# Performance work log

Hardware: AMD Instinct MI355X
Metric: run time of the kernel (lower is better)

Reference implementation:

```python
import jax, jax.numpy as jnp
import numpy as np

D = 768      # embed_dim
L = 8        # depth
NH = 4       # num_heads
HD = D // NH # head_dim = 192
GS = 16      # grid size (max_grid_size)
S = GS * GS  # 256 tokens
B = 64
EPS = 1.1920929e-07  # torch.finfo(float32).eps (RMSNorm eps=None)


def rmsnorm(x):
    return x * jax.lax.rsqrt(jnp.mean(x * x, axis=-1, keepdims=True) + EPS)


def householder_Q(vs):
    # sequential chain of Householder reflections: Q <- Q - (2/||v||^2) v (v^T Q)
    def step(Q, v):
        v = v[:, None]
        Q = Q - (2.0 / (jnp.sum(v * v) + 1e-08)) * (v @ (v.T @ Q))
        return Q, None
    Q, _ = jax.lax.scan(step, jnp.eye(vs.shape[1], dtype=vs.dtype), vs)
    return Q


def setup_inputs() -> dict:
    key = jax.random.key(0)
    ks = jax.random.split(key, 16)
    r = lambda k, shape, s=0.02: jax.random.normal(k, shape, jnp.float32) * s
    return dict(
        z_t=jax.random.normal(ks[0], (B, 3, 32, 32), jnp.float32),
        logsnr=jax.random.normal(ks[1], (B,), jnp.float32),
        qkv_w=r(ks[2], (L, D, 3 * D)),
        out_w=r(ks[3], (L, D, D)),
        gate_w=r(ks[4], (L, D, D)), gate_b=jnp.zeros((L, D), jnp.float32),
        mlpg_w=r(ks[5], (L, D, 8 * D)), mlpg_b=jnp.zeros((L, 8 * D), jnp.float32),
        mlpo_w=r(ks[6], (L, 4 * D, D)), mlpo_b=jnp.zeros((L, D), jnp.float32),
        hh_vs=r(ks[7], (L, HD // 2, HD)),
        patch_w=r(ks[8], (20, D)), patch_b=jnp.zeros((D,), jnp.float32),
        head_w=r(ks[9], (D, 12)), head_b=jnp.zeros((12,), jnp.float32),
        sd1_w=r(ks[10], (8, D)), sd1_b=jnp.zeros((D,), jnp.float32),
        sd2_w=r(ks[11], (D, 12)), sd2_b=jnp.zeros((12,), jnp.float32),
        lam_w=r(ks[12], (D, 1)), lam_b=jnp.zeros((1,), jnp.float32),
    )


def reference(z_t, logsnr, qkv_w, out_w, gate_w, gate_b, mlpg_w, mlpg_b,
              mlpo_w, mlpo_b, hh_vs, patch_w, patch_b, head_w, head_b,
              sd1_w, sd1_b, sd2_w, sd2_b, lam_w, lam_b):
    Bn, C, Him, Wim = z_t.shape
    gh = Him // 2
    # patchify 2x2 -> [B, S, 12]
    patches = z_t.reshape(Bn, C, gh, 2, gh, 2).transpose(0, 2, 4, 1, 3, 5).reshape(Bn, S, 12)
    # FourierFeatures(num_bands=4) -> 8-dim sin/cos embedding of logsnr
    bands = 2.0 ** jnp.arange(4, dtype=jnp.float32)
    ang = logsnr[:, None] * bands
    spins = jnp.concatenate([jnp.sin(ang), jnp.cos(ang)], axis=-1)  # [B, 8]
    x = jnp.concatenate([patches, jnp.broadcast_to(spins[:, None, :], (Bn, S, 8))], axis=-1) @ patch_w + patch_b

    # 2D RoPE tables on the 16x16 grid
    yy, xx = jnp.meshgrid(jnp.arange(GS), jnp.arange(GS), indexing='ij')
    coords = jnp.stack([yy.ravel(), xx.ravel()], axis=1).astype(jnp.float32)  # [S, 2]
    dim_half = HD // 2
    inv_freq = 1.0 / 10000.0 ** (jnp.arange(0, dim_half, 2, dtype=jnp.float32) / dim_half)
    fy = coords[:, 0:1] * inv_freq
    fx = coords[:, 1:2] * inv_freq
    emb = jnp.concatenate([fy, fx, fy, fx], axis=-1)  # [S, HD]
    cos, sin = jnp.cos(emb), jnp.sin(emb)

    # local sliding-window mask: euclidean distance on grid < 2.5
    d2 = jnp.sum((coords[:, None, :] - coords[None, :, :]) ** 2, axis=-1)
    local_mask = d2 < 2.5 ** 2  # [S, S]
    is_glob = jnp.array([(i + 1) % 4 == 0 for i in range(L)])
    scale = 1.0 / jnp.sqrt(jnp.float32(HD))

    def layer(x, p):
        qw, ow, gw, gb, mgw, mgb, mow, mob, vs, glob = p
        h = rmsnorm(x)
        q, k, v = jnp.split(h @ qw, 3, axis=-1)
        heads = lambda t: t.reshape(Bn, S, NH, HD).transpose(0, 2, 1, 3)  # [B,H,S,hd]
        q, k, v = heads(q), heads(k), heads(v)
        # RnRoPE: inverse Householder -> rotate -> forward Householder
        Q = householder_Q(vs)
        q, k = q @ Q.T, k @ Q.T
        def rot(t):
            t1, t2 = jnp.split(t, 2, axis=-1)
            return t * cos + jnp.concatenate([-t2, t1], axis=-1) * sin
        q, k = rot(q) @ Q, rot(k) @ Q
        scores = jnp.einsum('bhqd,bhkd->bhqk', q, k) * scale
        keep = local_mask | glob  # global layers attend everywhere
        scores = jnp.where(keep, scores, -1e30)
        attn = jax.nn.softmax(scores, axis=-1) @ v  # [B,H,S,hd]
        attn = attn.transpose(0, 2, 1, 3).reshape(Bn, S, D) @ ow
        gate = jax.nn.sigmoid(attn @ gw + gb)
        x = x + attn * gate
        g, val = jnp.split(rmsnorm(x) @ mgw + mgb, 2, axis=-1)
        x = x + (val * jax.nn.gelu(g, approximate=False)) @ mow + mob
        return x, None

    x, _ = jax.lax.scan(layer, x, (qkv_w, out_w, gate_w, gate_b, mlpg_w, mlpg_b,
                                   mlpo_w, mlpo_b, hh_vs, is_glob))
    x = rmsnorm(x)
    z_pred = x @ head_w + head_b  # [B, S, 12]
    # factorized mode: FourierScaleDecoder scale and lambda head
    scale_f = jnp.exp(jax.nn.silu(spins @ sd1_w + sd1_b) @ sd2_w + sd2_b)  # [B, 12]
    z_pred = z_pred * scale_f[:, None, :]
    l_pred = (jnp.mean(x, axis=1) @ lam_w + lam_b)[:, 0]
    z_img = z_pred.reshape(Bn, gh, gh, 3, 2, 2).transpose(0, 3, 1, 4, 2, 5).reshape(Bn, C, Him, Wim)
    return z_img, l_pred
```

## Files before the change

kernel.cpp:

```cpp
#include <hip/hip_runtime.h>
#include <hip/hip_bf16.h>
#include <math.h>


#define DEV static __device__ __forceinline__

typedef float    f32x4 __attribute__((ext_vector_type(4)));
typedef short    s16x8 __attribute__((ext_vector_type(8)));
typedef unsigned short u16x8 __attribute__((ext_vector_type(8)));
typedef unsigned short u16x4 __attribute__((ext_vector_type(4)));

constexpr int Bb = 64, Ss = 256, Dd = 768, Ll = 8, NHh = 4, HDd = 192;
constexpr int M_TOK = Bb * Ss;
constexpr float EPS_RMS = 1.1920929e-07f;
constexpr float ATT_SCALE = 0.07216878364870322f;
constexpr size_t ARENA_K = (size_t)Bb * NHh * Ss * HDd;

constexpr size_t B_SPINS  = 0;
constexpr size_t B_SCALEF = 2048;
constexpr size_t B_QT     = 5120;
constexpr size_t B_COS    = B_QT + 1179648;
constexpr size_t B_SIN    = B_COS + 196608;
constexpr size_t B_G      = B_SIN + 196608;
constexpr size_t B_T      = B_G + 294912;
constexpr size_t B_AWY    = B_T + 294912;
constexpr size_t B_ROWLAM = B_AWY + 589824;
constexpr size_t B_X      = B_ROWLAM + 65536;
constexpr size_t B_H      = B_X + 50331648;
constexpr size_t B_PROJ   = B_H + 25165824;
constexpr size_t B_WEFFT  = B_PROJ + 25165824;
constexpr size_t B_OUTWT  = B_WEFFT + 28311552;
constexpr size_t B_GATEWT = B_OUTWT + 9437184;
constexpr size_t B_MLPGT  = B_GATEWT + 9437184;
constexpr size_t B_MLPOT  = B_MLPGT + 75497472;
constexpr size_t B_ARENA  = B_MLPOT + 37748736;

DEV float sigmoidf_(float x) { return 1.0f / (1.0f + expf(-x)); }
DEV float geluf_(float g)    { return 0.5f * g * (1.0f + erff(g * 0.7071067811865476f)); }
DEV unsigned short f2bf(float f) {
    union { float f; unsigned u; } a; a.f = f;
    unsigned u = a.u + 0x7fffu + ((a.u >> 16) & 1u);
    return (unsigned short)(u >> 16);
}
DEV float b2f(unsigned short u) {
    union { unsigned u; float f; } a; a.u = ((unsigned)u) << 16; return a.f;
}
DEV void gload16(const void* g, void* l) {
    __builtin_amdgcn_global_load_lds((const __attribute__((address_space(1))) void*)g,
                                     (__attribute__((address_space(3))) void*)l, 16, 0, 0);
}

DEV void xcd_chunk(int gx, int gy, int CX, int& bx, int& by) {
    int id = by * gx + bx;
    int c = id & 7;
    int s = id >> 3;
    int CY = gy >> 3;
    int subsz = CY * CX;
    int bxc = s / subsz;
    int r = s - bxc * subsz;
    int byl = r / CX;
    by = c * CY + byl;
    bx = bxc * CX + (r - byl * CX);
}

__global__ void spins_kernel(const float* __restrict__ logsnr, float* __restrict__ spins) {
    int b = threadIdx.x;
    if (b < 64) {
        float v = logsnr[b];
#pragma unroll
        for (int j = 0; j < 4; ++j) {
            float ang = v * (float)(1 << j);
            spins[b * 8 + j]     = sinf(ang);
            spins[b * 8 + 4 + j] = cosf(ang);
        }
    }
}

__global__ void rope_table_kernel(float* __restrict__ cosb, float* __restrict__ sinb) {
    int s = blockIdx.x, j = threadIdx.x;
    int y = s >> 4, x = s & 15;
    int base = j % 96;
    float coord, invf;
    if (base < 48) { invf = expf(-(float)base * (2.0f / 96.0f) * 9.210340371976184f); coord = (float)y; }
    else { int i = base - 48; invf = expf(-(float)i * (2.0f / 96.0f) * 9.210340371976184f); coord = (float)x; }
    float f = coord * invf, sv, cv;
    sincosf(f, &sv, &cv);
    cosb[s * 192 + j] = cv;
    sinb[s * 192 + j] = sv;
}

__global__ __launch_bounds__(256) void hh_gram_kernel(const float* __restrict__ hh_vs,
                                                      float* __restrict__ Gm) {
    __shared__ float Y[96][192];
    int l = blockIdx.x, t = threadIdx.x;
    const float4* src = (const float4*)(hh_vs + (size_t)l * 96 * 192);
    for (int i = t; i < 4608; i += 256) ((float4*)&Y[0][0])[i] = src[i];
    __syncthreads();
    for (int e = t; e < 9216; e += 256) {
        int i = e / 96, j = e - (e / 96) * 96;
        float acc = 0.f;
        for (int d = 0; d < 48; ++d) {
            float4 a = *(const float4*)&Y[i][d * 4];
            float4 b = *(const float4*)&Y[j][d * 4];
            acc += a.x * b.x + a.y * b.y + a.z * b.z + a.w * b.w;
        }
        Gm[(size_t)l * 9216 + e] = acc;
    }
}

__global__ __launch_bounds__(128) void hh_t_kernel(const float* __restrict__ Gm,
                                                   float* __restrict__ Tm) {
    __shared__ float G[96][96];
    __shared__ float Tt[96][96];
    int l = blockIdx.x, t = threadIdx.x;
    const float* Gl = Gm + (size_t)l * 9216;
    for (int i = t; i < 9216; i += 128) { ((float*)G)[i] = Gl[i]; ((float*)Tt)[i] = 0.f; }
    __syncthreads();
    if (t < 96) Tt[t][t] = 2.0f / (G[t][t] + 1e-8f);
    __syncthreads();
    for (int j = 1; j < 96; ++j) {
        if (t < 96) {
            float cj = 2.0f / (G[j][j] + 1e-8f);
            float dot = 0.f;
            for (int p = 0; p < j; ++p) dot += Tt[p][t] * G[p][j];
            if (t < j) Tt[j][t] = -cj * dot;
        }
        __syncthreads();
    }
    for (int i = t; i < 9216; i += 128) Tm[(size_t)l * 9216 + i] = ((float*)Tt)[i];
}

__global__ __launch_bounds__(256) void hh_a_kernel(const float* __restrict__ Tm,
                                                   const float* __restrict__ hh_vs,
                                                   float* __restrict__ Am) {
    __shared__ float T[96][96];
    __shared__ float Y[96][192];
    int l = blockIdx.x, t = threadIdx.x;
    const float* Tl = Tm + (size_t)l * 9216;
    const float4* src = (const float4*)(hh_vs + (size_t)l * 96 * 192);
    for (int i = t; i < 9216; i += 256) ((float*)T)[i] = Tl[i];
    for (int i = t; i < 4608; i += 256) ((float4*)&Y[0][0])[i] = src[i];
    __syncthreads();
    for (int idx = t; idx < 4608; idx += 256) {
        int i = idx / 48, e0 = (idx % 48) * 4;
        float4 acc = {0.f, 0.f, 0.f, 0.f};
        for (int j = i; j < 96; ++j) {
            float tv = T[j][i];
            float4 y = *(const float4*)&Y[j][e0];
            acc.x += tv * y.x; acc.y += tv * y.y; acc.z += tv * y.z; acc.w += tv * y.w;
        }
        *(float4*)(Am + (size_t)l * 96 * 192 + (size_t)i * 192 + e0) = acc;
    }
}

__global__ __launch_bounds__(256) void hh_p_kernel(const float* __restrict__ hh_vs,
                                                   const float* __restrict__ Am,
                                                   float* __restrict__ qt) {
    __shared__ float Y[96][192];
    __shared__ float A[96][192];
    int l = blockIdx.x, t = threadIdx.x;
    const float4* ys = (const float4*)(hh_vs + (size_t)l * 96 * 192);
    const float4* as = (const float4*)(Am + (size_t)l * 96 * 192);
    for (int i = t; i < 4608; i += 256) { ((float4*)&Y[0][0])[i] = ys[i]; ((float4*)&A[0][0])[i] = as[i]; }
    __syncthreads();
    for (int idx = t; idx < 9216; idx += 256) {
        int d = idx / 48, e0 = (idx % 48) * 4;
        float4 acc = {0.f, 0.f, 0.f, 0.f};
        for (int i = 0; i < 96; ++i) {
            float yv = Y[i][d];
            float4 a = *(const float4*)&A[i][e0];
            acc.x += yv * a.x; acc.y += yv * a.y; acc.z += yv * a.z; acc.w += yv * a.w;
        }
        acc.x = (d == e0 + 0 ? 1.f : 0.f) - acc.x;
        acc.y = (d == e0 + 1 ? 1.f : 0.f) - acc.y;
        acc.z = (d == e0 + 2 ? 1.f : 0.f) - acc.z;
        acc.w = (d == e0 + 3 ? 1.f : 0.f) - acc.w;
        *(float4*)(qt + (size_t)l * 192 * 192 + (size_t)d * 192 + e0) = acc;
    }
}

__global__ __launch_bounds__(256) void fold_bf16t(const float* __restrict__ qkv_w,
                                                  const float* __restrict__ qt,
                                                  unsigned short* __restrict__ weff_t) {
    int z = blockIdx.z;
    int l = z >> 3, which = (z >> 2) & 1, head = z & 3;
    const float* A  = qkv_w + (size_t)l * 768 * 2304 + (size_t)which * 768 + head * 192;
    const float* Bq = qt + (size_t)l * 192 * 192;
    unsigned short* C = weff_t + (size_t)l * 2304 * 768 + ((size_t)which * 768 + head * 192) * 768;
    int row0 = blockIdx.y * 64, col0 = blockIdx.x * 64;
    __shared__ float As[64][65];
    __shared__ float Bs[64][65];
    int tid = threadIdx.x, tx = tid & 15, ty = tid >> 4;
    float acc[4][4] = {};
    for (int k0 = 0; k0 < 192; k0 += 64) {
        for (int i = tid; i < 1024; i += 256) {
            int r = i >> 4, kq = i & 15;
            float4 va = *(const float4*)(A + (size_t)(row0 + r) * 2304 + k0 + kq * 4);
            As[kq * 4 + 0][r] = va.x; As[kq * 4 + 1][r] = va.y; As[kq * 4 + 2][r] = va.z; As[kq * 4 + 3][r] = va.w;
        }
        for (int i = tid; i < 1024; i += 256) {
            int r = i >> 4, nq = i & 15;
            float4 vb = *(const float4*)(Bq + (size_t)(k0 + r) * 192 + col0 + nq * 4);
            Bs[r][nq * 4 + 0] = vb.x; Bs[r][nq * 4 + 1] = vb.y; Bs[r][nq * 4 + 2] = vb.z; Bs[r][nq * 4 + 3] = vb.w;
        }
        __syncthreads();
        for (int k = 0; k < 64; ++k) {
            float a[4], bb[4];
#pragma unroll
            for (int m = 0; m < 4; ++m) a[m] = As[k][ty * 4 + m];
#pragma unroll
            for (int n = 0; n < 4; ++n) bb[n] = Bs[k][tx * 4 + n];
#pragma unroll
            for (int m = 0; m < 4; ++m)
#pragma unroll
                for (int n = 0; n < 4; ++n) acc[m][n] = fmaf(a[m], bb[n], acc[m][n]);
        }
        __syncthreads();
    }
    float (*Tr)[65] = (float(*)[65])As;
#pragma unroll
    for (int m = 0; m < 4; ++m)
#pragma unroll
        for (int n = 0; n < 4; ++n) Tr[tx * 4 + n][ty * 4 + m] = acc[m][n];
    __syncthreads();
    int nl = tid >> 2, kc = (tid & 3) * 16;
#pragma unroll
    for (int q4 = 0; q4 < 4; ++q4) {
        u16x4 o;
#pragma unroll
        for (int ii = 0; ii < 4; ++ii) o[ii] = f2bf(Tr[nl][kc + q4 * 4 + ii]);
        *(u16x4*)(C + (size_t)(col0 + nl) * 768 + row0 + kc + q4 * 4) = o;
    }
}

__global__ __launch_bounds__(256) void transpose_bf16_kernel(const float* __restrict__ W,
                                                             int ldw, size_t zsrc,
                                                             unsigned short* __restrict__ Wt,
                                                             int ldwt, size_t zdst) {
    __shared__ float t[32][33];
    const float* Wz = W + (size_t)blockIdx.z * zsrc;
    unsigned short* Wtz = Wt + (size_t)blockIdx.z * zdst;
    int k0 = blockIdx.y * 32, n0 = blockIdx.x * 32;
    int tid = threadIdx.x;
    int tr = tid >> 3, tc = tid & 7;
    float4 v = *(const float4*)(Wz + (size_t)(k0 + tr) * ldw + n0 + tc * 4);
    t[tr][tc * 4 + 0] = v.x; t[tr][tc * 4 + 1] = v.y; t[tr][tc * 4 + 2] = v.z; t[tr][tc * 4 + 3] = v.w;
    __syncthreads();
    u16x4 o;
    o[0] = f2bf(t[tc * 4 + 0][tr]); o[1] = f2bf(t[tc * 4 + 1][tr]);
    o[2] = f2bf(t[tc * 4 + 2][tr]); o[3] = f2bf(t[tc * 4 + 3][tr]);
    *(u16x4*)(Wtz + (size_t)(n0 + tr) * ldwt + k0 + tc * 4) = o;
}

__global__ __launch_bounds__(256) void patch_embed_kernel(const float* __restrict__ z_t,
                                                          const float* __restrict__ spins,
                                                          const float* __restrict__ patch_w,
                                                          const float* __restrict__ patch_b,
                                                          float* __restrict__ x) {
    int bs = blockIdx.x;
    int b = bs >> 8, s = bs & 255;
    int gy = s >> 4, gx = s & 15;
    __shared__ float in20[20];
    int t = threadIdx.x;
    if (t < 12) {
        int c = t >> 2, py = (t >> 1) & 1, px = t & 1;
        in20[t] = z_t[(((size_t)b * 3 + c) * 32 + (2 * gy + py)) * 32 + (2 * gx + px)];
    } else if (t < 20) {
        in20[t] = spins[b * 8 + (t - 12)];
    }
    __syncthreads();
    for (int d = t; d < 768; d += 256) {
        float acc = patch_b[d];
#pragma unroll
        for (int i = 0; i < 20; ++i) acc += in20[i] * patch_w[i * 768 + d];
        x[(size_t)bs * 768 + d] = acc;
    }
}

__global__ __launch_bounds__(256) void rmsnorm_kernel(const float* __restrict__ x,
                                                      unsigned short* __restrict__ h) {
    int wave = threadIdx.x >> 6, lane = threadIdx.x & 63;
    int row = blockIdx.x * 4 + wave;
    const float* xr = x + (size_t)row * 768 + lane * 12;
    float4 a = *(const float4*)(xr);
    float4 b = *(const float4*)(xr + 4);
    float4 c = *(const float4*)(xr + 8);
    float ss = a.x*a.x + a.y*a.y + a.z*a.z + a.w*a.w
             + b.x*b.x + b.y*b.y + b.z*b.z + b.w*b.w
             + c.x*c.x + c.y*c.y + c.z*c.z + c.w*c.w;
#pragma unroll
    for (int msk = 1; msk < 64; msk <<= 1) ss += __shfl_xor(ss, msk);
    float sc = 1.0f / sqrtf(ss / 768.0f + EPS_RMS);
    unsigned short* hr = h + (size_t)row * 768 + lane * 12;
    u16x4 o0, o1, o2;
    o0[0]=f2bf(a.x*sc); o0[1]=f2bf(a.y*sc); o0[2]=f2bf(a.z*sc); o0[3]=f2bf(a.w*sc);
    o1[0]=f2bf(b.x*sc); o1[1]=f2bf(b.y*sc); o1[2]=f2bf(b.z*sc); o1[3]=f2bf(b.w*sc);
    o2[0]=f2bf(c.x*sc); o2[1]=f2bf(c.y*sc); o2[2]=f2bf(c.z*sc); o2[3]=f2bf(c.w*sc);
    *(u16x4*)(hr) = o0; *(u16x4*)(hr + 4) = o1; *(u16x4*)(hr + 8) = o2;
}

template <int EPI>
__global__ __launch_bounds__(256) void gemm_mfma(const unsigned short* __restrict__ A, int lda,
                                                 const unsigned short* __restrict__ Bt, int ldb,
                                                 unsigned short* __restrict__ Cb, int ldc, int K,
                                                 const float* __restrict__ bias,
                                                 float* __restrict__ Xf,
                                                 const unsigned short* __restrict__ Pb,
                                                 int CX) {
    __shared__ unsigned short As[4096];
    __shared__ unsigned short Bs[4096];
    int tid = threadIdx.x;
    int wave = tid >> 6, lane = tid & 63;
    int bx = blockIdx.x, by = blockIdx.y;
    xcd_chunk(gridDim.x, gridDim.y, CX, bx, by);
    int row0 = by * 128, col0 = bx * 128;
    int wm = wave >> 1, wn = wave & 1;
    f32x4 acc[4][4] = {};

    int srow = lane >> 2;
    int ksw = (((lane & 3) ^ (srow & 3)) * 8);
    int lrow = lane & 15;
    int csw = (((lane >> 4) ^ (lane & 3)) * 8);

    for (int k0 = 0; k0 < K; k0 += 32) {
#pragma unroll
        for (int it = 0; it < 2; ++it) {
            int chunk = it * 4 + wave;
            int r = chunk * 16 + srow;
            gload16(A  + (size_t)(row0 + r) * lda + k0 + ksw, &As[chunk * 512]);
            gload16(Bt + (size_t)(col0 + r) * ldb + k0 + ksw, &Bs[chunk * 512]);
        }
        __syncthreads();
        s16x8 af[4], bf[4];
#pragma unroll
        for (int m = 0; m < 4; ++m)
            af[m] = *(const s16x8*)&As[(wm * 64 + m * 16 + lrow) * 32 + csw];
#pragma unroll
        for (int n = 0; n < 4; ++n)
            bf[n] = *(const s16x8*)&Bs[(wn * 64 + n * 16 + lrow) * 32 + csw];
#pragma unroll
        for (int m = 0; m < 4; ++m)
#pragma unroll
            for (int n = 0; n < 4; ++n)
                acc[m][n] = __builtin_amdgcn_mfma_f32_16x16x32_bf16(af[m], bf[n], acc[m][n], 0, 0, 0);
        __syncthreads();
    }

    int lquad = lane >> 4;
#pragma unroll
    for (int m = 0; m < 4; ++m) {
#pragma unroll
        for (int n = 0; n < 4; ++n) {
#pragma unroll
            for (int r = 0; r < 4; ++r) {
                int i = row0 + wm * 64 + m * 16 + lquad * 4 + r;
                int j = col0 + wn * 64 + n * 16 + lrow;
                float v = acc[m][n][r];
                if (bias) v += bias[j];
                if constexpr (EPI == 0) {
                    Cb[(size_t)i * ldc + j] = f2bf(v);
                } else if constexpr (EPI == 1) {
                    int which = j / 768;
                    int rem = j - which * 768;
                    int head = rem / 192;
                    int hd = rem - head * 192;
                    int b = i >> 8, s = i & 255;
                    if (which == 2) {
                        Cb[2 * ARENA_K + (((size_t)(b * 4 + head)) * 192 + hd) * 256 + s] = f2bf(v);
                    } else {
                        Cb[(size_t)which * ARENA_K + (((size_t)(b * 4 + head)) * 256 + s) * 192 + hd] = f2bf(v);
                    }
                } else if constexpr (EPI == 2) {
                    float p = b2f(Pb[(size_t)i * 768 + j]);
                    Xf[(size_t)i * 768 + j] += p * sigmoidf_(v);
                } else if constexpr (EPI == 4) {
                    Xf[(size_t)i * ldc + j] += v;
                }
            }
        }
    }
}

__global__ __launch_bounds__(256) void gemm_mlp_fused(const unsigned short* __restrict__ A,
                                                      const unsigned short* __restrict__ Bt,
                                                      unsigned short* __restrict__ Hid,
                                                      const float* __restrict__ bias,
                                                      int CX) {
    __shared__ unsigned short As[4096];
    __shared__ unsigned short Bs[4096];
    int tid = threadIdx.x;
    int wave = tid >> 6, lane = tid & 63;
    int bx = blockIdx.x, by = blockIdx.y;
    xcd_chunk(gridDim.x, gridDim.y, CX, bx, by);
    int row0 = by * 128, col0 = bx * 64;
    int wm = wave >> 1, wn = wave & 1;
    f32x4 accg[4][2] = {};
    f32x4 accv[4][2] = {};

    int srow = lane >> 2;
    int ksw = (((lane & 3) ^ (srow & 3)) * 8);
    int lrow = lane & 15;
    int csw = (((lane >> 4) ^ (lane & 3)) * 8);

    const unsigned short* Bg = Bt + (size_t)col0 * 768;
    const unsigned short* Bv = Bt + (size_t)(3072 + col0) * 768;

    for (int k0 = 0; k0 < 768; k0 += 32) {
#pragma unroll
        for (int it = 0; it < 2; ++it) {
            int chunk = it * 4 + wave;
            int r = chunk * 16 + srow;
            gload16(A + (size_t)(row0 + r) * 768 + k0 + ksw, &As[chunk * 512]);
        }
        {
            int r = wave * 16 + srow;
            gload16(Bg + (size_t)r * 768 + k0 + ksw, &Bs[wave * 512]);
            gload16(Bv + (size_t)r * 768 + k0 + ksw, &Bs[2048 + wave * 512]);
        }
        __syncthreads();
        s16x8 af[4], bgf[2], bvf[2];
#pragma unroll
        for (int m = 0; m < 4; ++m)
            af[m] = *(const s16x8*)&As[(wm * 64 + m * 16 + lrow) * 32 + csw];
#pragma unroll
        for (int n = 0; n < 2; ++n) {
            bgf[n] = *(const s16x8*)&Bs[(wn * 32 + n * 16 + lrow) * 32 + csw];
            bvf[n] = *(const s16x8*)&Bs[2048 + (wn * 32 + n * 16 + lrow) * 32 + csw];
        }
#pragma unroll
        for (int m = 0; m < 4; ++m)
#pragma unroll
            for (int n = 0; n < 2; ++n) {
                accg[m][n] = __builtin_amdgcn_mfma_f32_16x16x32_bf16(af[m], bgf[n], accg[m][n], 0, 0, 0);
                accv[m][n] = __builtin_amdgcn_mfma_f32_16x16x32_bf16(af[m], bvf[n], accv[m][n], 0, 0, 0);
            }
        __syncthreads();
    }

    int lquad = lane >> 4;
#pragma unroll
    for (int m = 0; m < 4; ++m) {
#pragma unroll
        for (int n = 0; n < 2; ++n) {
#pragma unroll
            for (int r = 0; r < 4; ++r) {
                int i = row0 + wm * 64 + m * 16 + lquad * 4 + r;
                int j = col0 + wn * 32 + n * 16 + lrow;
                float g = accg[m][n][r] + bias[j];
                float v = accv[m][n][r] + bias[3072 + j];
                Hid[(size_t)i * 3072 + j] = f2bf(v * geluf_(g));
            }
        }
    }
}

__global__ __launch_bounds__(512) void attn_mfma_kernel(const unsigned short* __restrict__ qb_,
                                                        const unsigned short* __restrict__ kb_,
                                                        const unsigned short* __restrict__ vtb_,
                                                        unsigned short* __restrict__ attnb,
                                                        const float* __restrict__ cosb,
                                                        const float* __restrict__ sinb,
                                                        int glob) {
    __shared__ unsigned short Klds[256 * 200];
    __shared__ unsigned short Vlds[192 * 72];
    __shared__ unsigned short Plds[8 * 16 * 72];
    int b = blockIdx.z, hh = blockIdx.y;
    int tid = threadIdx.x;
    int wave = tid >> 6, lane = tid & 63;
    int q0 = blockIdx.x * 128 + wave * 16;
    size_t bh = (size_t)(b * 4 + hh);
    const unsigned short* qb  = qb_  + bh * 49152;
    const unsigned short* kb  = kb_  + bh * 49152;
    const unsigned short* vtb = vtb_ + bh * 49152;

    for (int c = tid; c < 6144; c += 512) {
        int r = c / 24, col = c - (c / 24) * 24;
        int j0 = col * 8;
        int jp = j0 < 96 ? j0 + 96 : j0 - 96;
        float sgn = j0 < 96 ? -1.f : 1.f;
        u16x8 a = *(const u16x8*)(kb + (size_t)r * 192 + j0);
        u16x8 p = *(const u16x8*)(kb + (size_t)r * 192 + jp);
        const float* cr = cosb + r * 192 + j0;
        const float* sr = sinb + r * 192 + j0;
        u16x8 o;
#pragma unroll
        for (int i = 0; i < 8; ++i)
            o[i] = f2bf(b2f(a[i]) * cr[i] + sgn * b2f(p[i]) * sr[i]);
        *(u16x8*)&Klds[r * 200 + j0] = o;
    }
    __syncthreads();

    s16x8 qf[6];
    {
        int sq = q0 + (lane & 15);
        const unsigned short* qrow = qb + (size_t)sq * 192;
        const float* cr = cosb + sq * 192;
        const float* sr = sinb + sq * 192;
#pragma unroll
        for (int kk = 0; kk < 6; ++kk) {
            int ck = kk * 32 + (lane >> 4) * 8;
            int cp = ck < 96 ? ck + 96 : ck - 96;
            float sgn = ck < 96 ? -1.f : 1.f;
            u16x8 a = *(const u16x8*)(qrow + ck);
            u16x8 p = *(const u16x8*)(qrow + cp);
            s16x8 o;
#pragma unroll
            for (int i = 0; i < 8; ++i)
                o[i] = (short)f2bf(b2f(a[i]) * cr[ck + i] + sgn * b2f(p[i]) * sr[ck + i]);
            qf[kk] = o;
        }
    }

    f32x4 sc[16];
#pragma unroll
    for (int n = 0; n < 16; ++n) sc[n] = (f32x4){0.f, 0.f, 0.f, 0.f};
#pragma unroll
    for (int kk = 0; kk < 6; ++kk) {
#pragma unroll
        for (int n = 0; n < 16; ++n) {
            s16x8 bf = *(const s16x8*)&Klds[(n * 16 + (lane & 15)) * 200 + kk * 32 + (lane >> 4) * 8];
            sc[n] = __builtin_amdgcn_mfma_f32_16x16x32_bf16(qf[kk], bf, sc[n], 0, 0, 0);
        }
    }

    int lq = (lane >> 4) * 4;
#pragma unroll
    for (int n = 0; n < 16; ++n) {
        int sk = n * 16 + (lane & 15);
        int yk = sk >> 4, xk = sk & 15;
#pragma unroll
        for (int r = 0; r < 4; ++r) {
            int sq = q0 + lq + r;
            int dy = (sq >> 4) - yk, dx = (sq & 15) - xk;
            bool keep = glob || (dy * dy + dx * dx) < 7;
            sc[n][r] = keep ? sc[n][r] * ATT_SCALE : -1e30f;
        }
    }
    float rmax[4], rsum[4];
#pragma unroll
    for (int r = 0; r < 4; ++r) {
        float m = sc[0][r];
#pragma unroll
        for (int n = 1; n < 16; ++n) m = fmaxf(m, sc[n][r]);
#pragma unroll
        for (int msk = 1; msk < 16; msk <<= 1) m = fmaxf(m, __shfl_xor(m, msk));
        rmax[r] = m;
    }
#pragma unroll
    for (int r = 0; r < 4; ++r) {
        float e = 0.f;
#pragma unroll
        for (int n = 0; n < 16; ++n) { float p = expf(sc[n][r] - rmax[r]); sc[n][r] = p; e += p; }
#pragma unroll
        for (int msk = 1; msk < 16; msk <<= 1) e += __shfl_xor(e, msk);
        rsum[r] = 1.0f / e;
    }

    f32x4 o[12];
#pragma unroll
    for (int n = 0; n < 12; ++n) o[n] = (f32x4){0.f, 0.f, 0.f, 0.f};
    unsigned short* Pw = &Plds[wave * 1152];
    for (int kt = 0; kt < 4; ++kt) {
#pragma unroll
        for (int nn = 0; nn < 4; ++nn) {
#pragma unroll
            for (int r = 0; r < 4; ++r)
                Pw[(lq + r) * 72 + nn * 16 + (lane & 15)] = f2bf(sc[kt * 4 + nn][r] * rsum[r]);
        }
        __syncthreads();
        for (int c = tid; c < 1536; c += 512) {
            int r = c >> 3, col = c & 7;
            *(u16x8*)&Vlds[r * 72 + col * 8] = *(const u16x8*)(vtb + (size_t)r * 256 + kt * 64 + col * 8);
        }
        __syncthreads();
        s16x8 af[2];
#pragma unroll
        for (int kk2 = 0; kk2 < 2; ++kk2)
            af[kk2] = *(const s16x8*)&Pw[(lane & 15) * 72 + kk2 * 32 + (lane >> 4) * 8];
#pragma unroll
        for (int n = 0; n < 12; ++n) {
#pragma unroll
            for (int kk2 = 0; kk2 < 2; ++kk2) {
                s16x8 bf = *(const s16x8*)&Vlds[(n * 16 + (lane & 15)) * 72 + kk2 * 32 + (lane >> 4) * 8];
                o[n] = __builtin_amdgcn_mfma_f32_16x16x32_bf16(af[kk2], bf, o[n], 0, 0, 0);
            }
        }
    }
#pragma unroll
    for (int n = 0; n < 12; ++n) {
        int d = n * 16 + (lane & 15);
#pragma unroll
        for (int r = 0; r < 4; ++r) {
            int sq = q0 + lq + r;
            attnb[((size_t)(b * 256 + sq)) * 768 + hh * 192 + d] = f2bf(o[n][r]);
        }
    }
}

__global__ __launch_bounds__(768) void scalef_kernel(const float* __restrict__ spins,
                                                     const float* __restrict__ sd1_w,
                                                     const float* __restrict__ sd1_b,
                                                     const float* __restrict__ sd2_w,
                                                     const float* __restrict__ sd2_b,
                                                     float* __restrict__ scalef) {
    int b = blockIdx.x, t = threadIdx.x;
    __shared__ float hid[768];
    __shared__ float sp[8];
    if (t < 8) sp[t] = spins[b * 8 + t];
    __syncthreads();
    float acc = sd1_b[t];
#pragma unroll
    for (int i = 0; i < 8; ++i) acc += sp[i] * sd1_w[i * 768 + t];
    hid[t] = acc * sigmoidf_(acc);
    __syncthreads();
    if (t < 12) {
        float o = sd2_b[t];
        for (int d = 0; d < 768; ++d) o += hid[d] * sd2_w[d * 12 + t];
        scalef[b * 12 + t] = expf(o);
    }
}

__global__ __launch_bounds__(256) void head_kernel(const unsigned short* __restrict__ xn,
                                                   const float* __restrict__ head_w,
                                                   const float* __restrict__ head_b,
                                                   const float* __restrict__ scalef,
                                                   const float* __restrict__ lam_w,
                                                   float* __restrict__ out,
                                                   float* __restrict__ rowlam) {
    __shared__ float hw[768][13];
    __shared__ float red[4][64][14];
    int t = threadIdx.x, wave = t >> 6, lane = t & 63;
    for (int i = t; i < 768 * 12; i += 256) hw[i / 12][i % 12] = head_w[i];
    for (int i = t; i < 768; i += 256) hw[i][12] = lam_w[i];
    __syncthreads();
    int row_base = blockIdx.x * 64;
    for (int rr = wave; rr < 64; rr += 4) {
        int row = row_base + rr;
        const unsigned short* xr = xn + (size_t)row * 768 + lane * 12;
        float xv[12];
        u16x4 v0 = *(const u16x4*)(xr);
        u16x4 v1 = *(const u16x4*)(xr + 4);
        u16x4 v2 = *(const u16x4*)(xr + 8);
#pragma unroll
        for (int j = 0; j < 4; ++j) { xv[j] = b2f(v0[j]); xv[4 + j] = b2f(v1[j]); xv[8 + j] = b2f(v2[j]); }
        float p[13] = {};
        int d0 = lane * 12;
#pragma unroll
        for (int dd = 0; dd < 12; ++dd) {
            float xvv = xv[dd];
#pragma unroll
            for (int o = 0; o < 12; ++o) p[o] += xvv * hw[d0 + dd][o];
            p[12] += xvv * hw[d0 + dd][12];
        }
#pragma unroll
        for (int o = 0; o < 13; ++o) red[wave][lane][o] = p[o];
        __syncthreads();
        if (lane < 13) {
            float s = 0.f;
            for (int i = 0; i < 64; ++i) s += red[wave][i][lane];
            if (lane < 12) {
                int b = row >> 8, sidx = row & 255;
                float v = (s + head_b[lane]) * scalef[b * 12 + lane];
                int c = lane >> 2, py = (lane >> 1) & 1, px = lane & 1;
                int gy = sidx >> 4, gxx = sidx & 15;
                out[(((size_t)b * 3 + c) * 32 + 2 * gy + py) * 32 + 2 * gxx + px] = v;
            } else {
                rowlam[row] = s;
            }
        }
        __syncthreads();
    }
}

__global__ __launch_bounds__(256) void lpred_kernel(const float* __restrict__ rowlam,
                                                    const float* __restrict__ lam_b,
                                                    float* __restrict__ out) {
    int b = blockIdx.x, t = threadIdx.x;
    __shared__ float red[256];
    red[t] = rowlam[b * 256 + t];
    __syncthreads();
    for (int s2 = 128; s2 > 0; s2 >>= 1) { if (t < s2) red[t] += red[t + s2]; __syncthreads(); }
    if (t == 0) out[196608 + b] = red[0] / 256.0f + lam_b[0];
}

extern "C" void kernel_launch(void* const* d_in, const int* in_sizes, int n_in,
                              void* d_out, int out_size, void* d_ws, size_t ws_size,
                              hipStream_t stream) {
    const float* z_t     = (const float*)d_in[0];
    const float* logsnr  = (const float*)d_in[1];
    const float* qkv_w   = (const float*)d_in[2];
    const float* out_w   = (const float*)d_in[3];
    const float* gate_w  = (const float*)d_in[4];
    const float* gate_b  = (const float*)d_in[5];
    const float* mlpg_w  = (const float*)d_in[6];
    const float* mlpg_b  = (const float*)d_in[7];
    const float* mlpo_w  = (const float*)d_in[8];
    const float* mlpo_b  = (const float*)d_in[9];
    const float* hh_vs   = (const float*)d_in[10];
    const float* patch_w = (const float*)d_in[11];
    const float* patch_b = (const float*)d_in[12];
    const float* head_w  = (const float*)d_in[13];
    const float* head_b  = (const float*)d_in[14];
    const float* sd1_w   = (const float*)d_in[15];
    const float* sd1_b   = (const float*)d_in[16];
    const float* sd2_w   = (const float*)d_in[17];
    const float* sd2_b   = (const float*)d_in[18];
    const float* lam_w   = (const float*)d_in[19];
    const float* lam_b   = (const float*)d_in[20];

    char* wsb = (char*)d_ws;
    float* spins  = (float*)(wsb + B_SPINS);
    float* scalef = (float*)(wsb + B_SCALEF);
    float* qt     = (float*)(wsb + B_QT);
    float* cosb   = (float*)(wsb + B_COS);
    float* sinb   = (float*)(wsb + B_SIN);
    float* Gm     = (float*)(wsb + B_G);
    float* Tm     = (float*)(wsb + B_T);
    float* Am     = (float*)(wsb + B_AWY);
    float* rowlam = (float*)(wsb + B_ROWLAM);
    float* x      = (float*)(wsb + B_X);
    unsigned short* h      = (unsigned short*)(wsb + B_H);
    unsigned short* proj   = (unsigned short*)(wsb + B_PROJ);
    unsigned short* weff_t = (unsigned short*)(wsb + B_WEFFT);
    unsigned short* outw_t = (unsigned short*)(wsb + B_OUTWT);
    unsigned short* gatew_t= (unsigned short*)(wsb + B_GATEWT);
    unsigned short* mlpg_t = (unsigned short*)(wsb + B_MLPGT);
    unsigned short* mlpo_t = (unsigned short*)(wsb + B_MLPOT);
    unsigned short* arena  = (unsigned short*)(wsb + B_ARENA);
    unsigned short* qbuf = arena;
    unsigned short* kbuf = arena + ARENA_K;
    unsigned short* vtbuf = arena + 2 * ARENA_K;
    unsigned short* attnb = arena + 3 * ARENA_K;
    unsigned short* hidden = arena;
    float* out = (float*)d_out;

    spins_kernel<<<1, 64, 0, stream>>>(logsnr, spins);
    rope_table_kernel<<<256, 192, 0, stream>>>(cosb, sinb);
    hh_gram_kernel<<<8, 256, 0, stream>>>(hh_vs, Gm);
    hh_t_kernel<<<8, 128, 0, stream>>>(Gm, Tm);
    hh_a_kernel<<<8, 256, 0, stream>>>(Tm, hh_vs, Am);
    hh_p_kernel<<<8, 256, 0, stream>>>(hh_vs, Am, qt);
    fold_bf16t<<<dim3(3, 12, 64), 256, 0, stream>>>(qkv_w, qt, weff_t);
    transpose_bf16_kernel<<<dim3(24, 24, 8), 256, 0, stream>>>(qkv_w + 1536, 2304,
        (size_t)768 * 2304, weff_t + (size_t)1536 * 768, 768, (size_t)2304 * 768);
    transpose_bf16_kernel<<<dim3(24, 24, 8), 256, 0, stream>>>(out_w, 768,
        (size_t)768 * 768, outw_t, 768, (size_t)768 * 768);
    transpose_bf16_kernel<<<dim3(24, 24, 8), 256, 0, stream>>>(gate_w, 768,
        (size_t)768 * 768, gatew_t, 768, (size_t)768 * 768);
    transpose_bf16_kernel<<<dim3(192, 24, 8), 256, 0, stream>>>(mlpg_w, 6144,
        (size_t)768 * 6144, mlpg_t, 768, (size_t)6144 * 768);
    transpose_bf16_kernel<<<dim3(24, 96, 8), 256, 0, stream>>>(mlpo_w, 768,
        (size_t)3072 * 768, mlpo_t, 3072, (size_t)768 * 3072);
    patch_embed_kernel<<<M_TOK, 256, 0, stream>>>(z_t, spins, patch_w, patch_b, x);

    for (int l = 0; l < Ll; ++l) {
        int glob = ((l + 1) % 4 == 0) ? 1 : 0;
        rmsnorm_kernel<<<4096, 256, 0, stream>>>(x, h);
        gemm_mfma<1><<<dim3(18, 128), 256, 0, stream>>>(h, 768,
            weff_t + (size_t)l * 2304 * 768, 768, arena, 0, 768, nullptr, nullptr, nullptr, 3);
        attn_mfma_kernel<<<dim3(2, 4, 64), 512, 0, stream>>>(qbuf, kbuf, vtbuf, attnb,
            cosb, sinb, glob);
        gemm_mfma<0><<<dim3(6, 128), 256, 0, stream>>>(attnb, 768,
            outw_t + (size_t)l * 768 * 768, 768, proj, 768, 768, nullptr, nullptr, nullptr, 3);
        gemm_mfma<2><<<dim3(6, 128), 256, 0, stream>>>(proj, 768,
            gatew_t + (size_t)l * 768 * 768, 768, nullptr, 768, 768,
            gate_b + (size_t)l * 768, x, proj, 3);
        rmsnorm_kernel<<<4096, 256, 0, stream>>>(x, h);
        gemm_mlp_fused<<<dim3(48, 128), 256, 0, stream>>>(h,
            mlpg_t + (size_t)l * 6144 * 768, hidden, mlpg_b + (size_t)l * 6144, 4);
        gemm_mfma<4><<<dim3(6, 128), 256, 0, stream>>>(hidden, 3072,
            mlpo_t + (size_t)l * 768 * 3072, 3072, nullptr, 768, 3072,
            mlpo_b + (size_t)l * 768, x, nullptr, 6);
    }

    rmsnorm_kernel<<<4096, 256, 0, stream>>>(x, h);
    scalef_kernel<<<64, 768, 0, stream>>>(spins, sd1_w, sd1_b, sd2_w, sd2_b, scalef);
    head_kernel<<<256, 256, 0, stream>>>(h, head_w, head_b, scalef, lam_w, out, rowlam);
    lpred_kernel<<<64, 256, 0, stream>>>(rowlam, lam_b, out);
}
```

Baseline: 5.918 ms.

## Double-buffer LDS tiles in MFMA GEMMs to overlap global loads with compute

Both bf16 MFMA GEMM kernels move from single-buffered to double-buffered LDS staging. The next K-tile's direct-to-LDS loads are issued before the current tile is computed, with explicit s_waitcnt vmcnt and raw s_barrier replacing __syncthreads. The goal is to hide global-memory latency behind MFMA work. In exchange, LDS use per block doubles, which may cut occupancy, and correctness now depends on the hand-written vmcnt counts matching the four loads issued per stage.

```diff
diff --git a/kernel.cpp b/kernel.cpp
--- a/kernel.cpp
+++ b/kernel.cpp
@@ -307,8 +307,8 @@
                                                  float* __restrict__ Xf,
                                                  const unsigned short* __restrict__ Pb,
                                                  int CX) {
-    __shared__ unsigned short As[4096];
-    __shared__ unsigned short Bs[4096];
+    __shared__ unsigned short As[2][4096];
+    __shared__ unsigned short Bs[2][4096];
     int tid = threadIdx.x;
     int wave = tid >> 6, lane = tid & 63;
     int bx = blockIdx.x, by = blockIdx.y;
@@ -322,28 +322,41 @@
     int lrow = lane & 15;
     int csw = (((lane >> 4) ^ (lane & 3)) * 8);
 
-    for (int k0 = 0; k0 < K; k0 += 32) {
+    auto stage = [&](int buf, int k0) {
 #pragma unroll
         for (int it = 0; it < 2; ++it) {
             int chunk = it * 4 + wave;
             int r = chunk * 16 + srow;
-            gload16(A  + (size_t)(row0 + r) * lda + k0 + ksw, &As[chunk * 512]);
-            gload16(Bt + (size_t)(col0 + r) * ldb + k0 + ksw, &Bs[chunk * 512]);
-        }
-        __syncthreads();
+            gload16(A  + (size_t)(row0 + r) * lda + k0 + ksw, &As[buf][chunk * 512]);
+            gload16(Bt + (size_t)(col0 + r) * ldb + k0 + ksw, &Bs[buf][chunk * 512]);
+        }
+    };
+
+    int NT = K >> 5;
+    stage(0, 0);
+    for (int t = 0; t < NT; ++t) {
+        if (t + 1 < NT) {
+            stage((t + 1) & 1, (t + 1) << 5);
+            asm volatile("s_waitcnt vmcnt(4)" ::: "memory");
+        } else {
+            asm volatile("s_waitcnt vmcnt(0)" ::: "memory");
+        }
+        __builtin_amdgcn_s_barrier();
+        const unsigned short* Ab = As[t & 1];
+        const unsigned short* Bb = Bs[t & 1];
         s16x8 af[4], bf[4];
 #pragma unroll
         for (int m = 0; m < 4; ++m)
-            af[m] = *(const s16x8*)&As[(wm * 64 + m * 16 + lrow) * 32 + csw];
+            af[m] = *(const s16x8*)&Ab[(wm * 64 + m * 16 + lrow) * 32 + csw];
 #pragma unroll
         for (int n = 0; n < 4; ++n)
-            bf[n] = *(const s16x8*)&Bs[(wn * 64 + n * 16 + lrow) * 32 + csw];
+            bf[n] = *(const s16x8*)&Bb[(wn * 64 + n * 16 + lrow) * 32 + csw];
 #pragma unroll
         for (int m = 0; m < 4; ++m)
 #pragma unroll
             for (int n = 0; n < 4; ++n)
                 acc[m][n] = __builtin_amdgcn_mfma_f32_16x16x32_bf16(af[m], bf[n], acc[m][n], 0, 0, 0);
-        __syncthreads();
+        __builtin_amdgcn_s_barrier();
     }
 
     int lquad = lane >> 4;
@@ -386,8 +399,8 @@
                                                       unsigned short* __restrict__ Hid,
                                                       const float* __restrict__ bias,
                                                       int CX) {
-    __shared__ unsigned short As[4096];
-    __shared__ unsigned short Bs[4096];
+    __shared__ unsigned short As[2][4096];
+    __shared__ unsigned short Bs[2][4096];
     int tid = threadIdx.x;
     int wave = tid >> 6, lane = tid & 63;
     int bx = blockIdx.x, by = blockIdx.y;
@@ -405,27 +418,39 @@
     const unsigned short* Bg = Bt + (size_t)col0 * 768;
     const unsigned short* Bv = Bt + (size_t)(3072 + col0) * 768;
 
-    for (int k0 = 0; k0 < 768; k0 += 32) {
+    auto stage = [&](int buf, int k0) {
 #pragma unroll
         for (int it = 0; it < 2; ++it) {
             int chunk = it * 4 + wave;
             int r = chunk * 16 + srow;
-            gload16(A + (size_t)(row0 + r) * 768 + k0 + ksw, &As[chunk * 512]);
+            gload16(A + (size_t)(row0 + r) * 768 + k0 + ksw, &As[buf][chunk * 512]);
         }
         {
             int r = wave * 16 + srow;
-            gload16(Bg + (size_t)r * 768 + k0 + ksw, &Bs[wave * 512]);
-            gload16(Bv + (size_t)r * 768 + k0 + ksw, &Bs[2048 + wave * 512]);
-        }
-        __syncthreads();
+            gload16(Bg + (size_t)r * 768 + k0 + ksw, &Bs[buf][wave * 512]);
+            gload16(Bv + (size_t)r * 768 + k0 + ksw, &Bs[buf][2048 + wave * 512]);
+        }
+    };
+
+    stage(0, 0);
+    for (int t = 0; t < 24; ++t) {
+        if (t + 1 < 24) {
+            stage((t + 1) & 1, (t + 1) << 5);
+            asm volatile("s_waitcnt vmcnt(4)" ::: "memory");
+        } else {
+            asm volatile("s_waitcnt vmcnt(0)" ::: "memory");
+        }
+        __builtin_amdgcn_s_barrier();
+        const unsigned short* Ab = As[t & 1];
+        const unsigned short* Bb = Bs[t & 1];
         s16x8 af[4], bgf[2], bvf[2];
 #pragma unroll
         for (int m = 0; m < 4; ++m)
-            af[m] = *(const s16x8*)&As[(wm * 64 + m * 16 + lrow) * 32 + csw];
+            af[m] = *(const s16x8*)&Ab[(wm * 64 + m * 16 + lrow) * 32 + csw];
 #pragma unroll
         for (int n = 0; n < 2; ++n) {
-            bgf[n] = *(const s16x8*)&Bs[(wn * 32 + n * 16 + lrow) * 32 + csw];
-            bvf[n] = *(const s16x8*)&Bs[2048 + (wn * 32 + n * 16 + lrow) * 32 + csw];
+            bgf[n] = *(const s16x8*)&Bb[(wn * 32 + n * 16 + lrow) * 32 + csw];
+            bvf[n] = *(const s16x8*)&Bb[2048 + (wn * 32 + n * 16 + lrow) * 32 + csw];
         }
 #pragma unroll
         for (int m = 0; m < 4; ++m)
@@ -434,7 +459,7 @@
                 accg[m][n] = __builtin_amdgcn_mfma_f32_16x16x32_bf16(af[m], bgf[n], accg[m][n], 0, 0, 0);
                 accv[m][n] = __builtin_amdgcn_mfma_f32_16x16x32_bf16(af[m], bvf[n], accv[m][n], 0, 0, 0);
             }
-        __syncthreads();
+        __builtin_amdgcn_s_barrier();
     }
 
     int lquad = lane >> 4;
```

Result: faster. 5.744 ms (-2.9%).
